# Kernel optimization log

Hardware: AMD Instinct MI355X
Metric: run time of the kernel (lower is better)

## Reference

```python
import jax, jax.numpy as jnp
import numpy as np

HID, FFN, E, K = 1024, 4096, 8, 2
CAP_FACTOR = 1.25


def setup_inputs() -> dict:
    key = jax.random.key(0)
    k1, k2, k3, k4 = jax.random.split(key, 4)
    B, T = 4, 2048
    x = jax.random.normal(k1, (B, T, HID), dtype=jnp.float32)
    router_w = jax.random.normal(k2, (E, HID), dtype=jnp.float32) * 0.02
    w1 = jax.random.normal(k3, (E, HID, FFN), dtype=jnp.float32) * 0.02
    w2 = jax.random.normal(k4, (E, FFN, HID), dtype=jnp.float32) * 0.02
    return {"x": x, "router_w": router_w, "w1": w1, "w2": w2}


def reference(x, router_w, w1, w2):
    B, T, H = x.shape
    N = B * T
    x_flat = x.reshape(N, H)
    # capacity per expert (static, shape-derived)
    C = max(1, int(CAP_FACTOR * N / E * K))

    # router (eval mode: no noise)
    logits = x_flat @ router_w.T                      # [N, E]
    probs = jax.nn.softmax(logits, axis=-1)
    top_v, top_i = jax.lax.top_k(probs, K)            # [N, K]
    top_v = top_v / jnp.sum(top_v, axis=-1, keepdims=True)

    out = jnp.zeros_like(x_flat)
    for k in range(K):
        eid = top_i[:, k]                             # [N] expert id per token
        gate = top_v[:, k]                            # [N]
        # position of each token within its expert, in token order
        onehot = jax.nn.one_hot(eid, E, dtype=jnp.int32)          # [N, E]
        pos = jnp.take_along_axis(jnp.cumsum(onehot, axis=0), eid[:, None], axis=1)[:, 0] - 1
        keep = pos < C                                # capacity drop (first C in token order)
        slot = jnp.where(keep, eid * C + pos, E * C)  # dropped tokens -> dump slot

        # dispatch: scatter kept tokens into per-expert capacity buffers
        buf = jnp.zeros((E * C + 1, H), dtype=x.dtype).at[slot].add(
            x_flat * keep[:, None].astype(x.dtype))
        expert_in = buf[: E * C].reshape(E, C, H)     # [E, C, H]

        # per-expert FFN (grouped GEMM -> GELU -> grouped GEMM)
        h = jax.nn.gelu(jnp.einsum('ech,ehf->ecf', expert_in, w1), approximate=False)
        y = jnp.einsum('ecf,efh->ech', h, w2)         # [E, C, H]

        # combine: gather back to token order, mask dropped, apply gate
        tok = y.reshape(E * C, H)[jnp.minimum(slot, E * C - 1)]
        out = out + tok * (gate * keep.astype(x.dtype))[:, None]

    return out.reshape(B, T, H)
```

## Files before the change

kernel.cpp:

```cpp
#include <hip/hip_runtime.h>
#include <hip/hip_bf16.h>
#include <math.h>

#define N_TOK 8192
#define HIDD  1024
#define FFND  4096
#define NE    8
#define CAP   2560
#define TMX   20
#define RMAX  16512

typedef __attribute__((ext_vector_type(4))) float  f32x4;
typedef __attribute__((ext_vector_type(8))) __bf16 bf16x8;

__device__ __forceinline__ unsigned short f2bf(float f) {
    unsigned u = __float_as_uint(f);
    u = (u + 0x7fffu + ((u >> 16) & 1u)) >> 16;
    return (unsigned short)u;
}

__device__ __forceinline__ void gld_lds16(const void* g, void* l) {
    __builtin_amdgcn_global_load_lds(
        (const __attribute__((address_space(1))) unsigned int*)g,
        (__attribute__((address_space(3))) unsigned int*)l, 16, 0, 0);
}

template <int R, int C>
__global__ __launch_bounds__(256) void transpose_cvt(const float* __restrict__ W,
                                                     unsigned short* __restrict__ Wt) {
    __shared__ unsigned short st[64][72];
    int e  = blockIdx.z;
    int r0 = blockIdx.y * 64, c0 = blockIdx.x * 64;
    int tid = threadIdx.x;
    int rb = tid >> 4, cq = tid & 15;
    const float* src = W + ((size_t)e * R + r0) * C + c0;
#pragma unroll
    for (int i = 0; i < 4; i++) {
        int kr = i * 16 + rb;
        float4 v = *reinterpret_cast<const float4*>(src + (size_t)kr * C + cq * 4);
        st[cq * 4 + 0][kr] = f2bf(v.x);
        st[cq * 4 + 1][kr] = f2bf(v.y);
        st[cq * 4 + 2][kr] = f2bf(v.z);
        st[cq * 4 + 3][kr] = f2bf(v.w);
    }
    __syncthreads();
    unsigned short* dst = Wt + ((size_t)e * C + c0) * R + r0;
#pragma unroll
    for (int i = 0; i < 4; i++) {
        int cr = i * 16 + rb;
        uint2 v = *reinterpret_cast<const uint2*>(&st[cr][cq * 4]);
        *reinterpret_cast<uint2*>(dst + (size_t)cr * R + cq * 4) = v;
    }
}

__global__ __launch_bounds__(256) void router_kernel(const float* __restrict__ x,
                                                     const float* __restrict__ rw,
                                                     unsigned short* __restrict__ xbf,
                                                     int* __restrict__ cnt,
                                                     int* __restrict__ tok,
                                                     float* __restrict__ gate) {
    __shared__ float4 rwl[2048];
    __shared__ int   e0s[32], e1s[32];
    __shared__ float g0s[32], g1s[32];
    __shared__ int   baseS[16];

    int tid = threadIdx.x, lane = tid & 63, w = tid >> 6;
    for (int i = tid; i < 2048; i += 256) rwl[i] = reinterpret_cast<const float4*>(rw)[i];
    __syncthreads();

    int tbase = blockIdx.x * 32 + w * 8;
    for (int i = 0; i < 8; i++) {
        int t = tbase + i;
        const float4* xr = reinterpret_cast<const float4*>(x) + (size_t)t * 256;
        float4 xv[4];
#pragma unroll
        for (int c = 0; c < 4; c++) xv[c] = xr[c * 64 + lane];
        uint2* xb = reinterpret_cast<uint2*>(xbf) + (size_t)t * 256;
#pragma unroll
        for (int c = 0; c < 4; c++) {
            uint2 p;
            p.x = (unsigned)f2bf(xv[c].x) | ((unsigned)f2bf(xv[c].y) << 16);
            p.y = (unsigned)f2bf(xv[c].z) | ((unsigned)f2bf(xv[c].w) << 16);
            xb[c * 64 + lane] = p;
        }
        float dot[NE];
#pragma unroll
        for (int e = 0; e < NE; e++) {
            float s = 0.f;
#pragma unroll
            for (int c = 0; c < 4; c++) {
                float4 a = rwl[e * 256 + c * 64 + lane];
                s += xv[c].x * a.x + xv[c].y * a.y + xv[c].z * a.z + xv[c].w * a.w;
            }
            dot[e] = s;
        }
#pragma unroll
        for (int e = 0; e < NE; e++) {
            float v = dot[e];
#pragma unroll
            for (int o = 32; o > 0; o >>= 1) v += __shfl_xor(v, o, 64);
            dot[e] = v;
        }
        if (lane == 0) {
            int e0 = 0; float l0 = dot[0];
#pragma unroll
            for (int e = 1; e < NE; e++) if (dot[e] > l0) { l0 = dot[e]; e0 = e; }
            int e1 = -1; float l1 = -3.4e38f;
#pragma unroll
            for (int e = 0; e < NE; e++) if (e != e0 && dot[e] > l1) { l1 = dot[e]; e1 = e; }
            float g0 = 1.f / (1.f + expf(l1 - l0));
            int j = w * 8 + i;
            e0s[j] = e0; e1s[j] = e1; g0s[j] = g0; g1s[j] = 1.f - g0;
        }
    }
    __syncthreads();

    int e0 = 255, e1 = 255, rank0 = 0, rank1 = 0, slotcnt = 0;
    float g0 = 0.f, g1 = 0.f;
    if (w == 0) {
        if (lane < 32) { e0 = e0s[lane]; e1 = e1s[lane]; g0 = g0s[lane]; g1 = g1s[lane]; }
        unsigned long long lt = (1ull << lane) - 1ull;
#pragma unroll
        for (int ee = 0; ee < NE; ee++) {
            unsigned long long m0 = __ballot(e0 == ee);
            unsigned long long m1 = __ballot(e1 == ee);
            if (e0 == ee) rank0 = (int)__popcll(m0 & lt);
            if (e1 == ee) rank1 = (int)__popcll(m1 & lt);
            if (lane == ee)      slotcnt = (int)__popcll(m0);
            if (lane == NE + ee) slotcnt = (int)__popcll(m1);
        }
        if (lane < 16) baseS[lane] = atomicAdd(&cnt[lane * 16], slotcnt);
    }
    __syncthreads();
    if (w == 0 && lane < 32) {
        int t = blockIdx.x * 32 + lane;
        int p0 = baseS[e0] + rank0;
        if (p0 < CAP) { tok[e0 * CAP + p0] = t; gate[e0 * CAP + p0] = g0; }
        int p1 = baseS[NE + e1] + rank1;
        if (p1 < CAP) { tok[(NE + e1) * CAP + p1] = t; gate[(NE + e1) * CAP + p1] = g1; }
    }
}

template <int KD, int ND, bool G1, int CH>
__global__ __launch_bounds__(256) void ffn_gemm_f(const unsigned short* __restrict__ A,
                                                  const unsigned short* __restrict__ Bw,
                                                  unsigned short* __restrict__ H,
                                                  float* __restrict__ O,
                                                  const int* __restrict__ cntAll,
                                                  const int* __restrict__ tokL,
                                                  const float* __restrict__ gateL) {
    constexpr int TN = ND / 128;
    int e = blockIdx.x & 7;
    int i = blockIdx.x >> 3;
    int cnt0 = min(cntAll[e * 16], CAP);
    int cnt1 = min(cntAll[(e + 8) * 16], CAP);
    int tmx0 = (cnt0 + 127) >> 7;
    int tmx1 = (cnt1 + 127) >> 7;
    int tmsum = tmx0 + tmx1;
    if (tmsum == 0) return;
    int per_chunk = tmsum * CH;
    int c = i / per_chunk;
    if (c >= TN / CH) return;
    int r = i - c * per_chunk;
    int s, tm, cnt_e;
    int t0 = tmx0 * CH;
    if (r < t0) { s = e;     tm = r / CH; r -= tm * CH; cnt_e = cnt0; }
    else { r -= t0; s = e + 8; tm = r / CH; r -= tm * CH; cnt_e = cnt1; }
    int tn = c * CH + r;

    int off_e = 0;
#pragma unroll
    for (int t = 0; t < 16; t++) off_e += (t < s) ? min(cntAll[t * 16], CAP) : 0;
    const int lbase = s * CAP;

    __shared__ __align__(16) unsigned short At[128 * 32];
    __shared__ __align__(16) unsigned short Bt[128 * 32];

    int tid = threadIdx.x;
    int w = tid >> 6, l = tid & 63;
    int wr = w >> 1, wc = w & 1;

    int r1 = tid >> 2, q1 = tid & 3;
    int r2 = r1 + 64;

    const char* aSrc1;
    const char* aSrc2;
    if (G1) {
        int p1 = tm * 128 + r1, p2 = tm * 128 + r2;
        int t1 = tokL[lbase + (p1 < cnt_e ? p1 : 0)];
        int t2 = tokL[lbase + (p2 < cnt_e ? p2 : 0)];
        aSrc1 = (const char*)(A + (size_t)t1 * KD) + ((q1 ^ ((r1 >> 1) & 3)) << 4);
        aSrc2 = (const char*)(A + (size_t)t2 * KD) + ((q1 ^ ((r2 >> 1) & 3)) << 4);
    } else {
        size_t row1 = (size_t)off_e + tm * 128 + r1;
        size_t row2 = row1 + 64;
        aSrc1 = (const char*)(A + row1 * KD) + ((q1 ^ ((r1 >> 1) & 3)) << 4);
        aSrc2 = (const char*)(A + row2 * KD) + ((q1 ^ ((r2 >> 1) & 3)) << 4);
    }
    const char* bSrc1 = (const char*)(Bw + ((size_t)e * ND + tn * 128 + r1) * KD) + ((q1 ^ ((r1 >> 1) & 3)) << 4);
    const char* bSrc2 = (const char*)(Bw + ((size_t)e * ND + tn * 128 + r2) * KD) + ((q1 ^ ((r2 >> 1) & 3)) << 4);

    char* aDst1 = (char*)At + w * 1024;
    char* aDst2 = aDst1 + 4096;
    char* bDst1 = (char*)Bt + w * 1024;
    char* bDst2 = bDst1 + 4096;

    int aro[4], bro[4];
#pragma unroll
    for (int m = 0; m < 4; m++) {
        int rr = wr * 64 + m * 16 + (l & 15);
        aro[m] = rr * 64 + (((l >> 4) ^ ((rr >> 1) & 3)) << 4);
        int cc = wc * 64 + m * 16 + (l & 15);
        bro[m] = cc * 64 + (((l >> 4) ^ ((cc >> 1) & 3)) << 4);
    }

    f32x4 zf = {0.f, 0.f, 0.f, 0.f};
    f32x4 acc[4][4];
#pragma unroll
    for (int m = 0; m < 4; m++)
#pragma unroll
        for (int n = 0; n < 4; n++) acc[m][n] = zf;

    for (int k0 = 0; k0 < KD; k0 += 32) {
        size_t kb = (size_t)k0 * 2;
        gld_lds16(aSrc1 + kb, aDst1);
        gld_lds16(aSrc2 + kb, aDst2);
        gld_lds16(bSrc1 + kb, bDst1);
        gld_lds16(bSrc2 + kb, bDst2);
        __syncthreads();
        bf16x8 af[4], bf[4];
#pragma unroll
        for (int m = 0; m < 4; m++) af[m] = *reinterpret_cast<const bf16x8*>((const char*)At + aro[m]);
#pragma unroll
        for (int n = 0; n < 4; n++) bf[n] = *reinterpret_cast<const bf16x8*>((const char*)Bt + bro[n]);
#pragma unroll
        for (int m = 0; m < 4; m++)
#pragma unroll
            for (int n = 0; n < 4; n++)
                acc[m][n] = __builtin_amdgcn_mfma_f32_16x16x32_bf16(af[m], bf[n], acc[m][n], 0, 0, 0);
        __syncthreads();
    }

    if (G1) {
#pragma unroll
        for (int m = 0; m < 4; m++) {
#pragma unroll
            for (int j = 0; j < 4; j++) {
                int rr = wr * 64 + m * 16 + (l >> 4) * 4 + j;
                int p = tm * 128 + rr;
                if (p < cnt_e) {
                    size_t row = (size_t)(off_e + p);
                    unsigned short* hp = H + row * ND + tn * 128 + wc * 64 + (l & 15);
#pragma unroll
                    for (int n = 0; n < 4; n++) {
                        float v = acc[m][n][j];
                        float g = 0.5f * v * (1.f + erff(v * 0.70710678118654752f));
                        hp[n * 16] = f2bf(g);
                    }
                }
            }
        }
    } else {
#pragma unroll
        for (int m = 0; m < 4; m++) {
#pragma unroll
            for (int j = 0; j < 4; j++) {
                int rr = wr * 64 + m * 16 + (l >> 4) * 4 + j;
                int p = tm * 128 + rr;
                if (p < cnt_e) {
                    int t = tokL[lbase + p];
                    float gv = gateL[lbase + p];
                    float* op = O + (size_t)t * ND + tn * 128 + wc * 64 + (l & 15);
#pragma unroll
                    for (int n = 0; n < 4; n++) atomicAdd(op + n * 16, gv * acc[m][n][j]);
                }
            }
        }
    }
}

template <int KD, int ND, bool G1>
__global__ __launch_bounds__(256) void ffn_gemm(const unsigned short* __restrict__ A,
                                                const float* __restrict__ W,
                                                unsigned short* __restrict__ H,
                                                float* __restrict__ O,
                                                const int* __restrict__ cntAll,
                                                const int* __restrict__ tokL,
                                                const float* __restrict__ gateL,
                                                int slot0, int pbase) {
    constexpr int TN = ND / 128;
    int bid = blockIdx.x;
    int tn  = bid % TN;
    int tme = bid / TN;
    int tm  = tme % TMX;
    int s   = slot0 + tme / TMX;
    int eW  = s & 7;
    int cnt_e = min(cntAll[s * 16], CAP);
    if (tm * 128 >= cnt_e) return;
    int off_e = 0;
#pragma unroll
    for (int i = 0; i < 16; i++) {
        int c = min(cntAll[i * 16], CAP);
        off_e += (i >= pbase && i < s) ? c : 0;
    }
    const int lbase = s * CAP;

    __shared__ __align__(16) unsigned short At[128 * 32];
    __shared__ __align__(16) unsigned short Bt[128 * 32];

    int tid = threadIdx.x;
    int w = tid >> 6, l = tid & 63;
    int wr = w >> 1, wc = w & 1;

    int r1 = tid >> 2, q1 = tid & 3;
    int r2 = r1 + 64;
    const char* aSrc1;
    const char* aSrc2;
    if (G1) {
        int p1 = tm * 128 + r1, p2 = tm * 128 + r2;
        int t1 = tokL[lbase + (p1 < cnt_e ? p1 : 0)];
        int t2 = tokL[lbase + (p2 < cnt_e ? p2 : 0)];
        aSrc1 = (const char*)(A + (size_t)t1 * KD) + ((q1 ^ ((r1 >> 1) & 3)) << 4);
        aSrc2 = (const char*)(A + (size_t)t2 * KD) + ((q1 ^ ((r2 >> 1) & 3)) << 4);
    } else {
        size_t row1 = (size_t)off_e + tm * 128 + r1;
        size_t row2 = row1 + 64;
        aSrc1 = (const char*)(A + row1 * KD) + ((q1 ^ ((r1 >> 1) & 3)) << 4);
        aSrc2 = (const char*)(A + row2 * KD) + ((q1 ^ ((r2 >> 1) & 3)) << 4);
    }
    char* aDst1 = (char*)At + w * 1024;
    char* aDst2 = aDst1 + 4096;

    const float* bSrc[4];
    int bOff[16];
#pragma unroll
    for (int j = 0; j < 4; j++) {
        int fidx = j * 1024 + tid * 4;
        int kk = fidx >> 7, n = fidx & 127;
        bSrc[j] = W + (size_t)eW * KD * ND + (size_t)kk * ND + tn * 128 + n;
#pragma unroll
        for (int i = 0; i < 4; i++) {
            int nn = n + i;
            bOff[j * 4 + i] = nn * 64 + ((((kk >> 3) ^ ((nn >> 1) & 3))) << 4) + ((kk & 7) << 1);
        }
    }

    int aro[4], bro[4];
#pragma unroll
    for (int m = 0; m < 4; m++) {
        int rr = wr * 64 + m * 16 + (l & 15);
        aro[m] = rr * 64 + (((l >> 4) ^ ((rr >> 1) & 3)) << 4);
        int cc = wc * 64 + m * 16 + (l & 15);
        bro[m] = cc * 64 + (((l >> 4) ^ ((cc >> 1) & 3)) << 4);
    }

    f32x4 zf = {0.f, 0.f, 0.f, 0.f};
    f32x4 acc[4][4];
#pragma unroll
    for (int m = 0; m < 4; m++)
#pragma unroll
        for (int n = 0; n < 4; n++) acc[m][n] = zf;

    for (int k0 = 0; k0 < KD; k0 += 32) {
        gld_lds16(aSrc1 + (size_t)k0 * 2, aDst1);
        gld_lds16(aSrc2 + (size_t)k0 * 2, aDst2);
        float4 bv[4];
#pragma unroll
        for (int j = 0; j < 4; j++) bv[j] = *reinterpret_cast<const float4*>(bSrc[j] + (size_t)k0 * ND);
        char* btc = (char*)Bt;
#pragma unroll
        for (int j = 0; j < 4; j++) {
            *(unsigned short*)(btc + bOff[j * 4 + 0]) = f2bf(bv[j].x);
            *(unsigned short*)(btc + bOff[j * 4 + 1]) = f2bf(bv[j].y);
            *(unsigned short*)(btc + bOff[j * 4 + 2]) = f2bf(bv[j].z);
            *(unsigned short*)(btc + bOff[j * 4 + 3]) = f2bf(bv[j].w);
        }
        __syncthreads();
        bf16x8 af[4], bf[4];
#pragma unroll
        for (int m = 0; m < 4; m++) af[m] = *reinterpret_cast<const bf16x8*>((const char*)At + aro[m]);
#pragma unroll
        for (int n = 0; n < 4; n++) bf[n] = *reinterpret_cast<const bf16x8*>((const char*)Bt + bro[n]);
#pragma unroll
        for (int m = 0; m < 4; m++)
#pragma unroll
            for (int n = 0; n < 4; n++)
                acc[m][n] = __builtin_amdgcn_mfma_f32_16x16x32_bf16(af[m], bf[n], acc[m][n], 0, 0, 0);
        __syncthreads();
    }

    if (G1) {
#pragma unroll
        for (int m = 0; m < 4; m++) {
#pragma unroll
            for (int j = 0; j < 4; j++) {
                int rr = wr * 64 + m * 16 + (l >> 4) * 4 + j;
                int p = tm * 128 + rr;
                if (p < cnt_e) {
                    size_t row = (size_t)(off_e + p);
                    unsigned short* hp = H + row * ND + tn * 128 + wc * 64 + (l & 15);
#pragma unroll
                    for (int n = 0; n < 4; n++) {
                        float v = acc[m][n][j];
                        float g = 0.5f * v * (1.f + erff(v * 0.70710678118654752f));
                        hp[n * 16] = f2bf(g);
                    }
                }
            }
        }
    } else {
#pragma unroll
        for (int m = 0; m < 4; m++) {
#pragma unroll
            for (int j = 0; j < 4; j++) {
                int rr = wr * 64 + m * 16 + (l >> 4) * 4 + j;
                int p = tm * 128 + rr;
                if (p < cnt_e) {
                    int t = tokL[lbase + p];
                    float gv = gateL[lbase + p];
                    float* op = O + (size_t)t * ND + tn * 128 + wc * 64 + (l & 15);
#pragma unroll
                    for (int n = 0; n < 4; n++) atomicAdd(op + n * 16, gv * acc[m][n][j]);
                }
            }
        }
    }
}

extern "C" void kernel_launch(void* const* d_in, const int* in_sizes, int n_in,
                              void* d_out, int out_size, void* d_ws, size_t ws_size,
                              hipStream_t stream) {
    const float* x  = (const float*)d_in[0];
    const float* rw = (const float*)d_in[1];
    const float* w1 = (const float*)d_in[2];
    const float* w2 = (const float*)d_in[3];
    float* out = (float*)d_out;
    char* ws = (char*)d_ws;

    int*   cnt  = (int*)ws;
    int*   tok  = (int*)(ws + 4096);
    float* gate = (float*)(ws + 4096 + 16 * CAP * 4);
    unsigned short* xbf = (unsigned short*)(ws + (1 << 20));
    size_t hOff = (1 << 20) + (size_t)N_TOK * HIDD * 2;
    unsigned short* h = (unsigned short*)(ws + hOff);

    size_t w1tSz = (size_t)NE * HIDD * FFND * 2;
    size_t hBig = (size_t)RMAX * FFND * 2;
    size_t needBig = hOff + hBig + 2 * w1tSz;

    hipMemsetAsync(cnt, 0, 1024, stream);
    hipMemsetAsync(d_out, 0, (size_t)N_TOK * HIDD * 4, stream);

    hipLaunchKernelGGL(router_kernel, dim3(N_TOK / 32), dim3(256), 0, stream,
                       x, rw, xbf, cnt, tok, gate);

    if (ws_size >= needBig) {
        unsigned short* w1t = (unsigned short*)(ws + hOff + hBig);
        unsigned short* w2t = (unsigned short*)(ws + hOff + hBig + w1tSz);
        hipLaunchKernelGGL((transpose_cvt<HIDD, FFND>), dim3(FFND / 64, HIDD / 64, NE), dim3(256), 0, stream, w1, w1t);
        hipLaunchKernelGGL((transpose_cvt<FFND, HIDD>), dim3(HIDD / 64, FFND / 64, NE), dim3(256), 0, stream, w2, w2t);
        hipLaunchKernelGGL((ffn_gemm_f<HIDD, FFND, true, 8>), dim3(8 * 2 * TMX * (FFND / 128)), dim3(256), 0, stream,
                           xbf, w1t, h, (float*)nullptr, cnt, tok, gate);
        hipLaunchKernelGGL((ffn_gemm_f<FFND, HIDD, false, 4>), dim3(8 * 2 * TMX * (HIDD / 128)), dim3(256), 0, stream,
                           h, w2t, (unsigned short*)nullptr, out, cnt, tok, gate);
    } else {
        for (int k = 0; k < 2; k++) {
            hipLaunchKernelGGL((ffn_gemm<HIDD, FFND, true>), dim3(8 * TMX * (FFND / 128)), dim3(256), 0, stream,
                               xbf, w1, h, (float*)nullptr, cnt, tok, gate, 8 * k, 8 * k);
            hipLaunchKernelGGL((ffn_gemm<FFND, HIDD, false>), dim3(8 * TMX * (HIDD / 128)), dim3(256), 0, stream,
                               h, w2, (unsigned short*)nullptr, out, cnt, tok, gate, 8 * k, 8 * k);
        }
    }
}
```

Baseline: 558.8 us.

## Replace expert GEMMs with 256-row tiled, double-buffered 8-wave kernel with split-K

```diff
diff --git a/kernel.cpp b/kernel.cpp
--- a/kernel.cpp
+++ b/kernel.cpp
@@ -8,6 +8,7 @@
 #define NE    8
 #define CAP   2560
 #define TMX   20
+#define TMX2  10
 #define RMAX  16512
 
 typedef __attribute__((ext_vector_type(4))) float  f32x4;
@@ -141,118 +142,183 @@
     }
 }
 
-template <int KD, int ND, bool G1, int CH>
-__global__ __launch_bounds__(256) void ffn_gemm_f(const unsigned short* __restrict__ A,
-                                                  const unsigned short* __restrict__ Bw,
-                                                  unsigned short* __restrict__ H,
-                                                  float* __restrict__ O,
-                                                  const int* __restrict__ cntAll,
-                                                  const int* __restrict__ tokL,
-                                                  const float* __restrict__ gateL) {
-    constexpr int TN = ND / 128;
+template <int KD, int ND, int BN, int KS, bool G1>
+__global__ __launch_bounds__(512, 2) void ffn_gemm8(const unsigned short* __restrict__ A,
+                                                    const unsigned short* __restrict__ Bw,
+                                                    unsigned short* __restrict__ H,
+                                                    float* __restrict__ O,
+                                                    const int* __restrict__ cntAll,
+                                                    const int* __restrict__ tokL,
+                                                    const float* __restrict__ gateL) {
+    constexpr int TN      = ND / BN;
+    constexpr int UNITS   = TN * KS;
+    constexpr int WAVES_M = G1 ? 2 : 4;
+    constexpr int WAVES_N = 8 / WAVES_M;
+    constexpr int M_REP   = 256 / (WAVES_M * 16);
+    constexpr int N_REP   = BN / (WAVES_N * 16);
+    constexpr int BSW     = BN / 64;
+    constexpr int KDS     = KD / KS;
+    constexpr int NT      = KDS / 64;
+    constexpr int LDSA    = 256 * 128;
+    constexpr int LDSB    = BN * 128;
+
+    extern __shared__ __align__(16) char smem[];
+
     int e = blockIdx.x & 7;
     int i = blockIdx.x >> 3;
     int cnt0 = min(cntAll[e * 16], CAP);
     int cnt1 = min(cntAll[(e + 8) * 16], CAP);
-    int tmx0 = (cnt0 + 127) >> 7;
-    int tmx1 = (cnt1 + 127) >> 7;
+    int tmx0 = (cnt0 + 255) >> 8, tmx1 = (cnt1 + 255) >> 8;
     int tmsum = tmx0 + tmx1;
     if (tmsum == 0) return;
-    int per_chunk = tmsum * CH;
+    int per_chunk = tmsum * 4;
     int c = i / per_chunk;
-    if (c >= TN / CH) return;
+    if (c >= UNITS / 4) return;
     int r = i - c * per_chunk;
     int s, tm, cnt_e;
-    int t0 = tmx0 * CH;
-    if (r < t0) { s = e;     tm = r / CH; r -= tm * CH; cnt_e = cnt0; }
-    else { r -= t0; s = e + 8; tm = r / CH; r -= tm * CH; cnt_e = cnt1; }
-    int tn = c * CH + r;
+    if (r < tmx0 * 4) { s = e;     tm = r >> 2; r &= 3; cnt_e = cnt0; }
+    else { r -= tmx0 * 4; s = e + 8; tm = r >> 2; r &= 3; cnt_e = cnt1; }
+    int u  = c * 4 + r;
+    int tn = u / KS, ks = (KS > 1) ? (u % KS) : 0;
 
     int off_e = 0;
 #pragma unroll
     for (int t = 0; t < 16; t++) off_e += (t < s) ? min(cntAll[t * 16], CAP) : 0;
     const int lbase = s * CAP;
 
-    __shared__ __align__(16) unsigned short At[128 * 32];
-    __shared__ __align__(16) unsigned short Bt[128 * 32];
-
     int tid = threadIdx.x;
-    int w = tid >> 6, l = tid & 63;
-    int wr = w >> 1, wc = w & 1;
-
-    int r1 = tid >> 2, q1 = tid & 3;
-    int r2 = r1 + 64;
-
-    const char* aSrc1;
-    const char* aSrc2;
+    int l = tid & 63, w = tid >> 6;
+
+    int srow = w * 8 + (l >> 3);
+    int swz  = (((l & 7) ^ ((l >> 3) & 7)) << 4);
+
+    int aoff[4];
+#pragma unroll
+    for (int j = 0; j < 4; j++) {
+        int p = tm * 256 + j * 64 + srow;
+        if (G1) {
+            int t = tokL[lbase + (p < cnt_e ? p : 0)];
+            aoff[j] = t * (KD * 2) + ks * (KDS * 2) + swz;
+        } else {
+            aoff[j] = (off_e + p) * (KD * 2) + ks * (KDS * 2) + swz;
+        }
+    }
+    int boff[BSW];
+#pragma unroll
+    for (int j = 0; j < BSW; j++) {
+        int nr = e * ND + tn * BN + j * 64 + srow;
+        boff[j] = nr * (KD * 2) + ks * (KDS * 2) + swz;
+    }
+    int dstoff = (w * 8) * 128;
+
+    int wm = G1 ? (w >> 2) : (w >> 1);
+    int wn = G1 ? (w & 3) : (w & 1);
+    int arow = wm * (256 / WAVES_M) + (l & 15);
+    int brow = wn * (BN / WAVES_N) + (l & 15);
+    int rsw  = (((l >> 4) ^ (l & 7)) << 4);
+    int aR[2], bR[2];
+    aR[0] = arow * 128 + rsw;  aR[1] = aR[0] ^ 64;
+    bR[0] = brow * 128 + rsw;  bR[1] = bR[0] ^ 64;
+
+    const char* Ab = (const char*)A;
+    const char* Bb = (const char*)Bw;
+
+    f32x4 acc[M_REP][N_REP];
+#pragma unroll
+    for (int m = 0; m < M_REP; m++)
+#pragma unroll
+        for (int n = 0; n < N_REP; n++) acc[m][n] = (f32x4){0.f, 0.f, 0.f, 0.f};
+
+#pragma unroll
+    for (int j = 0; j < 4; j++)   gld_lds16(Ab + aoff[j], smem + dstoff + j * 8192);
+#pragma unroll
+    for (int j = 0; j < BSW; j++) gld_lds16(Bb + boff[j], smem + LDSA + dstoff + j * 8192);
+#pragma unroll
+    for (int j = 0; j < 4; j++)   aoff[j] += 128;
+#pragma unroll
+    for (int j = 0; j < BSW; j++) boff[j] += 128;
+
+    bf16x8 afr[M_REP][2], bfr[N_REP][2];
+
+    for (int t = 0; t < NT - 1; t++) {
+        char* bufc = smem + (t & 1) * (LDSA + LDSB);
+        char* bufn = smem + ((t + 1) & 1) * (LDSA + LDSB);
+#pragma unroll
+        for (int j = 0; j < 4; j++) { gld_lds16(Ab + aoff[j], bufn + dstoff + j * 8192); aoff[j] += 128; }
+        asm volatile("s_waitcnt vmcnt(4)" ::: "memory");
+        __builtin_amdgcn_s_barrier();
+        asm volatile("" ::: "memory");
+#pragma unroll
+        for (int m = 0; m < M_REP; m++)
+#pragma unroll
+            for (int kk = 0; kk < 2; kk++)
+                afr[m][kk] = *reinterpret_cast<const bf16x8*>(bufc + aR[kk] + m * 2048);
+#pragma unroll
+        for (int n = 0; n < N_REP; n++)
+#pragma unroll
+            for (int kk = 0; kk < 2; kk++)
+                bfr[n][kk] = *reinterpret_cast<const bf16x8*>(bufc + LDSA + bR[kk] + n * 2048);
+        __builtin_amdgcn_s_setprio(1);
+#pragma unroll
+        for (int m = 0; m < M_REP; m++)
+#pragma unroll
+            for (int n = 0; n < N_REP; n++)
+                acc[m][n] = __builtin_amdgcn_mfma_f32_16x16x32_bf16(afr[m][0], bfr[n][0], acc[m][n], 0, 0, 0);
+        __builtin_amdgcn_s_setprio(0);
+#pragma unroll
+        for (int j = 0; j < BSW; j++) { gld_lds16(Bb + boff[j], bufn + LDSA + dstoff + j * 8192); boff[j] += 128; }
+        asm volatile("s_waitcnt lgkmcnt(0)" ::: "memory");
+        __builtin_amdgcn_sched_barrier(0);
+        __builtin_amdgcn_s_barrier();
+        asm volatile("" ::: "memory");
+        __builtin_amdgcn_s_setprio(1);
+#pragma unroll
+        for (int m = 0; m < M_REP; m++)
+#pragma unroll
+            for (int n = 0; n < N_REP; n++)
+                acc[m][n] = __builtin_amdgcn_mfma_f32_16x16x32_bf16(afr[m][1], bfr[n][1], acc[m][n], 0, 0, 0);
+        __builtin_amdgcn_s_setprio(0);
+    }
+    {
+        char* bufc = smem + ((NT - 1) & 1) * (LDSA + LDSB);
+        asm volatile("s_waitcnt vmcnt(0)" ::: "memory");
+        __builtin_amdgcn_s_barrier();
+        asm volatile("" ::: "memory");
+#pragma unroll
+        for (int m = 0; m < M_REP; m++)
+#pragma unroll
+            for (int kk = 0; kk < 2; kk++)
+                afr[m][kk] = *reinterpret_cast<const bf16x8*>(bufc + aR[kk] + m * 2048);
+#pragma unroll
+        for (int n = 0; n < N_REP; n++)
+#pragma unroll
+            for (int kk = 0; kk < 2; kk++)
+                bfr[n][kk] = *reinterpret_cast<const bf16x8*>(bufc + LDSA + bR[kk] + n * 2048);
+        __builtin_amdgcn_s_setprio(1);
+#pragma unroll
+        for (int m = 0; m < M_REP; m++)
+#pragma unroll
+            for (int n = 0; n < N_REP; n++)
+                acc[m][n] = __builtin_amdgcn_mfma_f32_16x16x32_bf16(afr[m][0], bfr[n][0], acc[m][n], 0, 0, 0);
+#pragma unroll
+        for (int m = 0; m < M_REP; m++)
+#pragma unroll
+            for (int n = 0; n < N_REP; n++)
+                acc[m][n] = __builtin_amdgcn_mfma_f32_16x16x32_bf16(afr[m][1], bfr[n][1], acc[m][n], 0, 0, 0);
+        __builtin_amdgcn_s_setprio(0);
+    }
+
     if (G1) {
-        int p1 = tm * 128 + r1, p2 = tm * 128 + r2;
-        int t1 = tokL[lbase + (p1 < cnt_e ? p1 : 0)];
-        int t2 = tokL[lbase + (p2 < cnt_e ? p2 : 0)];
-        aSrc1 = (const char*)(A + (size_t)t1 * KD) + ((q1 ^ ((r1 >> 1) & 3)) << 4);
-        aSrc2 = (const char*)(A + (size_t)t2 * KD) + ((q1 ^ ((r2 >> 1) & 3)) << 4);
-    } else {
-        size_t row1 = (size_t)off_e + tm * 128 + r1;
-        size_t row2 = row1 + 64;
-        aSrc1 = (const char*)(A + row1 * KD) + ((q1 ^ ((r1 >> 1) & 3)) << 4);
-        aSrc2 = (const char*)(A + row2 * KD) + ((q1 ^ ((r2 >> 1) & 3)) << 4);
-    }
-    const char* bSrc1 = (const char*)(Bw + ((size_t)e * ND + tn * 128 + r1) * KD) + ((q1 ^ ((r1 >> 1) & 3)) << 4);
-    const char* bSrc2 = (const char*)(Bw + ((size_t)e * ND + tn * 128 + r2) * KD) + ((q1 ^ ((r2 >> 1) & 3)) << 4);
-
-    char* aDst1 = (char*)At + w * 1024;
-    char* aDst2 = aDst1 + 4096;
-    char* bDst1 = (char*)Bt + w * 1024;
-    char* bDst2 = bDst1 + 4096;
-
-    int aro[4], bro[4];
-#pragma unroll
-    for (int m = 0; m < 4; m++) {
-        int rr = wr * 64 + m * 16 + (l & 15);
-        aro[m] = rr * 64 + (((l >> 4) ^ ((rr >> 1) & 3)) << 4);
-        int cc = wc * 64 + m * 16 + (l & 15);
-        bro[m] = cc * 64 + (((l >> 4) ^ ((cc >> 1) & 3)) << 4);
-    }
-
-    f32x4 zf = {0.f, 0.f, 0.f, 0.f};
-    f32x4 acc[4][4];
-#pragma unroll
-    for (int m = 0; m < 4; m++)
-#pragma unroll
-        for (int n = 0; n < 4; n++) acc[m][n] = zf;
-
-    for (int k0 = 0; k0 < KD; k0 += 32) {
-        size_t kb = (size_t)k0 * 2;
-        gld_lds16(aSrc1 + kb, aDst1);
-        gld_lds16(aSrc2 + kb, aDst2);
-        gld_lds16(bSrc1 + kb, bDst1);
-        gld_lds16(bSrc2 + kb, bDst2);
-        __syncthreads();
-        bf16x8 af[4], bf[4];
-#pragma unroll
-        for (int m = 0; m < 4; m++) af[m] = *reinterpret_cast<const bf16x8*>((const char*)At + aro[m]);
-#pragma unroll
-        for (int n = 0; n < 4; n++) bf[n] = *reinterpret_cast<const bf16x8*>((const char*)Bt + bro[n]);
-#pragma unroll
-        for (int m = 0; m < 4; m++)
-#pragma unroll
-            for (int n = 0; n < 4; n++)
-                acc[m][n] = __builtin_amdgcn_mfma_f32_16x16x32_bf16(af[m], bf[n], acc[m][n], 0, 0, 0);
-        __syncthreads();
-    }
-
-    if (G1) {
-#pragma unroll
-        for (int m = 0; m < 4; m++) {
+#pragma unroll
+        for (int m = 0; m < M_REP; m++) {
 #pragma unroll
             for (int j = 0; j < 4; j++) {
-                int rr = wr * 64 + m * 16 + (l >> 4) * 4 + j;
-                int p = tm * 128 + rr;
+                int rr = wm * (256 / WAVES_M) + m * 16 + (l >> 4) * 4 + j;
+                int p = tm * 256 + rr;
                 if (p < cnt_e) {
-                    size_t row = (size_t)(off_e + p);
-                    unsigned short* hp = H + row * ND + tn * 128 + wc * 64 + (l & 15);
-#pragma unroll
-                    for (int n = 0; n < 4; n++) {
+                    unsigned short* hp = H + (size_t)(off_e + p) * ND + tn * BN + wn * (BN / WAVES_N) + (l & 15);
+#pragma unroll
+                    for (int n = 0; n < N_REP; n++) {
                         float v = acc[m][n][j];
                         float g = 0.5f * v * (1.f + erff(v * 0.70710678118654752f));
                         hp[n * 16] = f2bf(g);
@@ -262,17 +328,17 @@
         }
     } else {
 #pragma unroll
-        for (int m = 0; m < 4; m++) {
+        for (int m = 0; m < M_REP; m++) {
 #pragma unroll
             for (int j = 0; j < 4; j++) {
-                int rr = wr * 64 + m * 16 + (l >> 4) * 4 + j;
-                int p = tm * 128 + rr;
+                int rr = wm * (256 / WAVES_M) + m * 16 + (l >> 4) * 4 + j;
+                int p = tm * 256 + rr;
                 if (p < cnt_e) {
                     int t = tokL[lbase + p];
                     float gv = gateL[lbase + p];
-                    float* op = O + (size_t)t * ND + tn * 128 + wc * 64 + (l & 15);
-#pragma unroll
-                    for (int n = 0; n < 4; n++) atomicAdd(op + n * 16, gv * acc[m][n][j]);
+                    float* op = O + (size_t)t * ND + tn * BN + wn * (BN / WAVES_N) + (l & 15);
+#pragma unroll
+                    for (int n = 0; n < N_REP; n++) atomicAdd(op + n * 16, gv * acc[m][n][j]);
                 }
             }
         }
@@ -459,9 +525,11 @@
         unsigned short* w2t = (unsigned short*)(ws + hOff + hBig + w1tSz);
         hipLaunchKernelGGL((transpose_cvt<HIDD, FFND>), dim3(FFND / 64, HIDD / 64, NE), dim3(256), 0, stream, w1, w1t);
         hipLaunchKernelGGL((transpose_cvt<FFND, HIDD>), dim3(HIDD / 64, FFND / 64, NE), dim3(256), 0, stream, w2, w2t);
-        hipLaunchKernelGGL((ffn_gemm_f<HIDD, FFND, true, 8>), dim3(8 * 2 * TMX * (FFND / 128)), dim3(256), 0, stream,
+        hipLaunchKernelGGL((ffn_gemm8<HIDD, FFND, 256, 1, true>), dim3(8 * 2 * TMX2 * 16), dim3(512),
+                           2 * (256 * 128 + 256 * 128), stream,
                            xbf, w1t, h, (float*)nullptr, cnt, tok, gate);
-        hipLaunchKernelGGL((ffn_gemm_f<FFND, HIDD, false, 4>), dim3(8 * 2 * TMX * (HIDD / 128)), dim3(256), 0, stream,
+        hipLaunchKernelGGL((ffn_gemm8<FFND, HIDD, 128, 2, false>), dim3(8 * 2 * TMX2 * 16), dim3(512),
+                           2 * (256 * 128 + 128 * 128), stream,
                            h, w2t, (unsigned short*)nullptr, out, cnt, tok, gate);
     } else {
         for (int k = 0; k < 2; k++) {
```

Result: slower. 578.0 us (+3.4%).

## Use 256x128 tiles with triple-buffered async LDS pipeline and split-K

Applied to the files above, without the earlier changes.

```diff
diff --git a/kernel.cpp b/kernel.cpp
--- a/kernel.cpp
+++ b/kernel.cpp
@@ -141,116 +141,151 @@
     }
 }
 
-template <int KD, int ND, bool G1, int CH>
-__global__ __launch_bounds__(256) void ffn_gemm_f(const unsigned short* __restrict__ A,
-                                                  const unsigned short* __restrict__ Bw,
-                                                  unsigned short* __restrict__ H,
-                                                  float* __restrict__ O,
-                                                  const int* __restrict__ cntAll,
-                                                  const int* __restrict__ tokL,
-                                                  const float* __restrict__ gateL) {
-    constexpr int TN = ND / 128;
+template <int KD, int ND, int KS, bool G1>
+__global__ __launch_bounds__(512, 2) void ffn_gemm8(const unsigned short* __restrict__ A,
+                                                    const unsigned short* __restrict__ Bw,
+                                                    unsigned short* __restrict__ H,
+                                                    float* __restrict__ O,
+                                                    const int* __restrict__ cntAll,
+                                                    const int* __restrict__ tokL,
+                                                    const float* __restrict__ gateL) {
+    constexpr int TN    = ND / 128;
+    constexpr int UNITS = TN * KS;
+    constexpr int CH    = G1 ? 8 : 4;
+    constexpr int KDS   = KD / KS;
+    constexpr int NT    = KDS / 64;
+    constexpr int LDSA  = 256 * 128;
+    constexpr int LDSB  = 128 * 128;
+    constexpr int BUF   = LDSA + LDSB;
+
+    extern __shared__ __align__(16) char smem[];
+
     int e = blockIdx.x & 7;
     int i = blockIdx.x >> 3;
     int cnt0 = min(cntAll[e * 16], CAP);
     int cnt1 = min(cntAll[(e + 8) * 16], CAP);
-    int tmx0 = (cnt0 + 127) >> 7;
-    int tmx1 = (cnt1 + 127) >> 7;
+    int tmx0 = (cnt0 + 255) >> 8, tmx1 = (cnt1 + 255) >> 8;
     int tmsum = tmx0 + tmx1;
     if (tmsum == 0) return;
     int per_chunk = tmsum * CH;
     int c = i / per_chunk;
-    if (c >= TN / CH) return;
+    if (c >= UNITS / CH) return;
     int r = i - c * per_chunk;
     int s, tm, cnt_e;
-    int t0 = tmx0 * CH;
-    if (r < t0) { s = e;     tm = r / CH; r -= tm * CH; cnt_e = cnt0; }
-    else { r -= t0; s = e + 8; tm = r / CH; r -= tm * CH; cnt_e = cnt1; }
-    int tn = c * CH + r;
+    if (r < tmx0 * CH) { s = e;     tm = r / CH; r -= tm * CH; cnt_e = cnt0; }
+    else { r -= tmx0 * CH; s = e + 8; tm = r / CH; r -= tm * CH; cnt_e = cnt1; }
+    int u  = c * CH + r;
+    int tn = (KS > 1) ? (u / KS) : u;
+    int ks = (KS > 1) ? (u % KS) : 0;
 
     int off_e = 0;
 #pragma unroll
     for (int t = 0; t < 16; t++) off_e += (t < s) ? min(cntAll[t * 16], CAP) : 0;
     const int lbase = s * CAP;
 
-    __shared__ __align__(16) unsigned short At[128 * 32];
-    __shared__ __align__(16) unsigned short Bt[128 * 32];
-
     int tid = threadIdx.x;
-    int w = tid >> 6, l = tid & 63;
-    int wr = w >> 1, wc = w & 1;
-
-    int r1 = tid >> 2, q1 = tid & 3;
-    int r2 = r1 + 64;
-
-    const char* aSrc1;
-    const char* aSrc2;
-    if (G1) {
-        int p1 = tm * 128 + r1, p2 = tm * 128 + r2;
-        int t1 = tokL[lbase + (p1 < cnt_e ? p1 : 0)];
-        int t2 = tokL[lbase + (p2 < cnt_e ? p2 : 0)];
-        aSrc1 = (const char*)(A + (size_t)t1 * KD) + ((q1 ^ ((r1 >> 1) & 3)) << 4);
-        aSrc2 = (const char*)(A + (size_t)t2 * KD) + ((q1 ^ ((r2 >> 1) & 3)) << 4);
-    } else {
-        size_t row1 = (size_t)off_e + tm * 128 + r1;
-        size_t row2 = row1 + 64;
-        aSrc1 = (const char*)(A + row1 * KD) + ((q1 ^ ((r1 >> 1) & 3)) << 4);
-        aSrc2 = (const char*)(A + row2 * KD) + ((q1 ^ ((r2 >> 1) & 3)) << 4);
-    }
-    const char* bSrc1 = (const char*)(Bw + ((size_t)e * ND + tn * 128 + r1) * KD) + ((q1 ^ ((r1 >> 1) & 3)) << 4);
-    const char* bSrc2 = (const char*)(Bw + ((size_t)e * ND + tn * 128 + r2) * KD) + ((q1 ^ ((r2 >> 1) & 3)) << 4);
-
-    char* aDst1 = (char*)At + w * 1024;
-    char* aDst2 = aDst1 + 4096;
-    char* bDst1 = (char*)Bt + w * 1024;
-    char* bDst2 = bDst1 + 4096;
-
-    int aro[4], bro[4];
-#pragma unroll
-    for (int m = 0; m < 4; m++) {
-        int rr = wr * 64 + m * 16 + (l & 15);
-        aro[m] = rr * 64 + (((l >> 4) ^ ((rr >> 1) & 3)) << 4);
-        int cc = wc * 64 + m * 16 + (l & 15);
-        bro[m] = cc * 64 + (((l >> 4) ^ ((cc >> 1) & 3)) << 4);
-    }
-
-    f32x4 zf = {0.f, 0.f, 0.f, 0.f};
+    int l = tid & 63, w = tid >> 6;
+
+    int srow = w * 8 + (l >> 3);
+    int swz  = (((l & 7) ^ ((l >> 3) & 7)) << 4);
+
+    int aoff[4];
+#pragma unroll
+    for (int j = 0; j < 4; j++) {
+        int p = tm * 256 + j * 64 + srow;
+        if (G1) {
+            int t = tokL[lbase + (p < cnt_e ? p : 0)];
+            aoff[j] = t * (KD * 2) + ks * (KDS * 2) + swz;
+        } else {
+            aoff[j] = (off_e + p) * (KD * 2) + ks * (KDS * 2) + swz;
+        }
+    }
+    int boff[2];
+#pragma unroll
+    for (int j = 0; j < 2; j++) {
+        int nr = e * ND + tn * 128 + j * 64 + srow;
+        boff[j] = nr * (KD * 2) + ks * (KDS * 2) + swz;
+    }
+    int adst = w * 1024;
+
+    const char* Ab = (const char*)A;
+    const char* Bb = (const char*)Bw;
+
+    int wm = w >> 1, wn = w & 1;
+    int arow = wm * 64 + (l & 15);
+    int brow = wn * 64 + (l & 15);
+    int rsw  = (((l >> 4) ^ (l & 7)) << 4);
+    int aR0 = arow * 128 + rsw;
+    int bR0 = brow * 128 + rsw;
+
     f32x4 acc[4][4];
 #pragma unroll
     for (int m = 0; m < 4; m++)
 #pragma unroll
-        for (int n = 0; n < 4; n++) acc[m][n] = zf;
-
-    for (int k0 = 0; k0 < KD; k0 += 32) {
-        size_t kb = (size_t)k0 * 2;
-        gld_lds16(aSrc1 + kb, aDst1);
-        gld_lds16(aSrc2 + kb, aDst2);
-        gld_lds16(bSrc1 + kb, bDst1);
-        gld_lds16(bSrc2 + kb, bDst2);
-        __syncthreads();
+        for (int n = 0; n < 4; n++) acc[m][n] = (f32x4){0.f, 0.f, 0.f, 0.f};
+
+    char* b0 = smem;
+    char* b1 = smem + BUF;
+    char* b2 = smem + 2 * BUF;
+
+#define STAGE_A(buf) do { _Pragma("unroll") \
+    for (int j = 0; j < 4; j++) { gld_lds16(Ab + aoff[j], (buf) + adst + j * 8192); aoff[j] += 128; } } while (0)
+#define STAGE_B(buf) do { _Pragma("unroll") \
+    for (int j = 0; j < 2; j++) { gld_lds16(Bb + boff[j], (buf) + LDSA + adst + j * 8192); boff[j] += 128; } } while (0)
+
+    STAGE_A(b0); STAGE_B(b0);
+    STAGE_A(b1); STAGE_B(b1);
+    asm volatile("s_waitcnt vmcnt(6)" ::: "memory");
+    __builtin_amdgcn_s_barrier();
+    asm volatile("" ::: "memory");
+
+    for (int t = 0; t < NT; t++) {
+        bool pf = (t + 2 < NT);
         bf16x8 af[4], bf[4];
 #pragma unroll
-        for (int m = 0; m < 4; m++) af[m] = *reinterpret_cast<const bf16x8*>((const char*)At + aro[m]);
-#pragma unroll
-        for (int n = 0; n < 4; n++) bf[n] = *reinterpret_cast<const bf16x8*>((const char*)Bt + bro[n]);
+        for (int m = 0; m < 4; m++) af[m] = *reinterpret_cast<const bf16x8*>(b0 + aR0 + m * 2048);
+#pragma unroll
+        for (int n = 0; n < 4; n++) bf[n] = *reinterpret_cast<const bf16x8*>(b0 + LDSA + bR0 + n * 2048);
+        if (pf) STAGE_A(b2);
+        __builtin_amdgcn_s_setprio(1);
 #pragma unroll
         for (int m = 0; m < 4; m++)
 #pragma unroll
             for (int n = 0; n < 4; n++)
                 acc[m][n] = __builtin_amdgcn_mfma_f32_16x16x32_bf16(af[m], bf[n], acc[m][n], 0, 0, 0);
-        __syncthreads();
-    }
+        __builtin_amdgcn_s_setprio(0);
+#pragma unroll
+        for (int m = 0; m < 4; m++) af[m] = *reinterpret_cast<const bf16x8*>(b0 + (aR0 ^ 64) + m * 2048);
+#pragma unroll
+        for (int n = 0; n < 4; n++) bf[n] = *reinterpret_cast<const bf16x8*>(b0 + LDSA + (bR0 ^ 64) + n * 2048);
+        if (pf) STAGE_B(b2);
+        __builtin_amdgcn_s_setprio(1);
+#pragma unroll
+        for (int m = 0; m < 4; m++)
+#pragma unroll
+            for (int n = 0; n < 4; n++)
+                acc[m][n] = __builtin_amdgcn_mfma_f32_16x16x32_bf16(af[m], bf[n], acc[m][n], 0, 0, 0);
+        __builtin_amdgcn_s_setprio(0);
+        if (pf) asm volatile("s_waitcnt vmcnt(6)" ::: "memory");
+        else    asm volatile("s_waitcnt vmcnt(0)" ::: "memory");
+        if (t + 1 < NT) {
+            __builtin_amdgcn_s_barrier();
+            asm volatile("" ::: "memory");
+        }
+        char* bt = b0; b0 = b1; b1 = b2; b2 = bt;
+    }
+#undef STAGE_A
+#undef STAGE_B
 
     if (G1) {
 #pragma unroll
         for (int m = 0; m < 4; m++) {
 #pragma unroll
             for (int j = 0; j < 4; j++) {
-                int rr = wr * 64 + m * 16 + (l >> 4) * 4 + j;
-                int p = tm * 128 + rr;
+                int rr = wm * 64 + m * 16 + (l >> 4) * 4 + j;
+                int p = tm * 256 + rr;
                 if (p < cnt_e) {
-                    size_t row = (size_t)(off_e + p);
-                    unsigned short* hp = H + row * ND + tn * 128 + wc * 64 + (l & 15);
+                    unsigned short* hp = H + (size_t)(off_e + p) * ND + tn * 128 + wn * 64 + (l & 15);
 #pragma unroll
                     for (int n = 0; n < 4; n++) {
                         float v = acc[m][n][j];
@@ -265,12 +300,12 @@
         for (int m = 0; m < 4; m++) {
 #pragma unroll
             for (int j = 0; j < 4; j++) {
-                int rr = wr * 64 + m * 16 + (l >> 4) * 4 + j;
-                int p = tm * 128 + rr;
+                int rr = wm * 64 + m * 16 + (l >> 4) * 4 + j;
+                int p = tm * 256 + rr;
                 if (p < cnt_e) {
                     int t = tokL[lbase + p];
                     float gv = gateL[lbase + p];
-                    float* op = O + (size_t)t * ND + tn * 128 + wc * 64 + (l & 15);
+                    float* op = O + (size_t)t * ND + tn * 128 + wn * 64 + (l & 15);
 #pragma unroll
                     for (int n = 0; n < 4; n++) atomicAdd(op + n * 16, gv * acc[m][n][j]);
                 }
@@ -459,10 +494,11 @@
         unsigned short* w2t = (unsigned short*)(ws + hOff + hBig + w1tSz);
         hipLaunchKernelGGL((transpose_cvt<HIDD, FFND>), dim3(FFND / 64, HIDD / 64, NE), dim3(256), 0, stream, w1, w1t);
         hipLaunchKernelGGL((transpose_cvt<FFND, HIDD>), dim3(HIDD / 64, FFND / 64, NE), dim3(256), 0, stream, w2, w2t);
-        hipLaunchKernelGGL((ffn_gemm_f<HIDD, FFND, true, 8>), dim3(8 * 2 * TMX * (FFND / 128)), dim3(256), 0, stream,
-                           xbf, w1t, h, (float*)nullptr, cnt, tok, gate);
-        hipLaunchKernelGGL((ffn_gemm_f<FFND, HIDD, false, 4>), dim3(8 * 2 * TMX * (HIDD / 128)), dim3(256), 0, stream,
-                           h, w2t, (unsigned short*)nullptr, out, cnt, tok, gate);
+        constexpr int SMEM = 3 * (256 * 128 + 128 * 128);
+        hipLaunchKernelGGL((ffn_gemm8<HIDD, FFND, 1, true>), dim3(8 * 20 * 32), dim3(512),
+                           SMEM, stream, xbf, w1t, h, (float*)nullptr, cnt, tok, gate);
+        hipLaunchKernelGGL((ffn_gemm8<FFND, HIDD, 2, false>), dim3(8 * 20 * 16), dim3(512),
+                           SMEM, stream, h, w2t, (unsigned short*)nullptr, out, cnt, tok, gate);
     } else {
         for (int k = 0; k < 2; k++) {
             hipLaunchKernelGGL((ffn_gemm<HIDD, FFND, true>), dim3(8 * TMX * (FFND / 128)), dim3(256), 0, stream,
```

New measurement: 572.1 us. 2.4% more time.

## Use persistent per-expert GEMM blocks and split-K for the second FFN GEMM

Applied to the files above, without the earlier changes.

```diff
diff --git a/kernel.cpp b/kernel.cpp
--- a/kernel.cpp
+++ b/kernel.cpp
@@ -9,6 +9,7 @@
 #define CAP   2560
 #define TMX   20
 #define RMAX  16512
+#define PBLK  128
 
 typedef __attribute__((ext_vector_type(4))) float  f32x4;
 typedef __attribute__((ext_vector_type(8))) __bf16 bf16x8;
@@ -141,40 +142,39 @@
     }
 }
 
-template <int KD, int ND, bool G1, int CH>
-__global__ __launch_bounds__(256) void ffn_gemm_f(const unsigned short* __restrict__ A,
-                                                  const unsigned short* __restrict__ Bw,
-                                                  unsigned short* __restrict__ H,
-                                                  float* __restrict__ O,
-                                                  const int* __restrict__ cntAll,
-                                                  const int* __restrict__ tokL,
-                                                  const float* __restrict__ gateL) {
-    constexpr int TN = ND / 128;
-    int e = blockIdx.x & 7;
-    int i = blockIdx.x >> 3;
+template <int KD, int ND, int KS, int CH, bool G1>
+__global__ __launch_bounds__(256, 4) void ffn_gemm_p(const unsigned short* __restrict__ A,
+                                                     const unsigned short* __restrict__ Bw,
+                                                     unsigned short* __restrict__ H,
+                                                     float* __restrict__ O,
+                                                     const int* __restrict__ cntAll,
+                                                     const int* __restrict__ tokL,
+                                                     const float* __restrict__ gateL) {
+    constexpr int TN    = ND / 128;
+    constexpr int UNITS = TN * KS;
+    constexpr int KDS   = KD / KS;
+
+    __shared__ __align__(16) unsigned short At[128 * 32];
+    __shared__ __align__(16) unsigned short Bt[128 * 32];
+
+    int e  = blockIdx.x & 7;
+    int pb = blockIdx.x >> 3;
+
     int cnt0 = min(cntAll[e * 16], CAP);
     int cnt1 = min(cntAll[(e + 8) * 16], CAP);
-    int tmx0 = (cnt0 + 127) >> 7;
-    int tmx1 = (cnt1 + 127) >> 7;
+    int tmx0 = (cnt0 + 127) >> 7, tmx1 = (cnt1 + 127) >> 7;
     int tmsum = tmx0 + tmx1;
     if (tmsum == 0) return;
     int per_chunk = tmsum * CH;
-    int c = i / per_chunk;
-    if (c >= TN / CH) return;
-    int r = i - c * per_chunk;
-    int s, tm, cnt_e;
-    int t0 = tmx0 * CH;
-    if (r < t0) { s = e;     tm = r / CH; r -= tm * CH; cnt_e = cnt0; }
-    else { r -= t0; s = e + 8; tm = r / CH; r -= tm * CH; cnt_e = cnt1; }
-    int tn = c * CH + r;
-
-    int off_e = 0;
-#pragma unroll
-    for (int t = 0; t < 16; t++) off_e += (t < s) ? min(cntAll[t * 16], CAP) : 0;
-    const int lbase = s * CAP;
-
-    __shared__ __align__(16) unsigned short At[128 * 32];
-    __shared__ __align__(16) unsigned short Bt[128 * 32];
+    int total = tmsum * UNITS;
+
+    int offA = 0, offB = 0;
+#pragma unroll
+    for (int t = 0; t < 16; t++) {
+        int cc = min(cntAll[t * 16], CAP);
+        if (t < e)     offA += cc;
+        if (t < e + 8) offB += cc;
+    }
 
     int tid = threadIdx.x;
     int w = tid >> 6, l = tid & 63;
@@ -182,24 +182,8 @@
 
     int r1 = tid >> 2, q1 = tid & 3;
     int r2 = r1 + 64;
-
-    const char* aSrc1;
-    const char* aSrc2;
-    if (G1) {
-        int p1 = tm * 128 + r1, p2 = tm * 128 + r2;
-        int t1 = tokL[lbase + (p1 < cnt_e ? p1 : 0)];
-        int t2 = tokL[lbase + (p2 < cnt_e ? p2 : 0)];
-        aSrc1 = (const char*)(A + (size_t)t1 * KD) + ((q1 ^ ((r1 >> 1) & 3)) << 4);
-        aSrc2 = (const char*)(A + (size_t)t2 * KD) + ((q1 ^ ((r2 >> 1) & 3)) << 4);
-    } else {
-        size_t row1 = (size_t)off_e + tm * 128 + r1;
-        size_t row2 = row1 + 64;
-        aSrc1 = (const char*)(A + row1 * KD) + ((q1 ^ ((r1 >> 1) & 3)) << 4);
-        aSrc2 = (const char*)(A + row2 * KD) + ((q1 ^ ((r2 >> 1) & 3)) << 4);
-    }
-    const char* bSrc1 = (const char*)(Bw + ((size_t)e * ND + tn * 128 + r1) * KD) + ((q1 ^ ((r1 >> 1) & 3)) << 4);
-    const char* bSrc2 = (const char*)(Bw + ((size_t)e * ND + tn * 128 + r2) * KD) + ((q1 ^ ((r2 >> 1) & 3)) << 4);
-
+    int sw1 = ((q1 ^ ((r1 >> 1) & 3)) << 4);
+    int sw2 = ((q1 ^ ((r2 >> 1) & 3)) << 4);
     char* aDst1 = (char*)At + w * 1024;
     char* aDst2 = aDst1 + 4096;
     char* bDst1 = (char*)Bt + w * 1024;
@@ -214,65 +198,91 @@
         bro[m] = cc * 64 + (((l >> 4) ^ ((cc >> 1) & 3)) << 4);
     }
 
-    f32x4 zf = {0.f, 0.f, 0.f, 0.f};
-    f32x4 acc[4][4];
-#pragma unroll
-    for (int m = 0; m < 4; m++)
-#pragma unroll
-        for (int n = 0; n < 4; n++) acc[m][n] = zf;
-
-    for (int k0 = 0; k0 < KD; k0 += 32) {
-        size_t kb = (size_t)k0 * 2;
-        gld_lds16(aSrc1 + kb, aDst1);
-        gld_lds16(aSrc2 + kb, aDst2);
-        gld_lds16(bSrc1 + kb, bDst1);
-        gld_lds16(bSrc2 + kb, bDst2);
-        __syncthreads();
-        bf16x8 af[4], bf[4];
-#pragma unroll
-        for (int m = 0; m < 4; m++) af[m] = *reinterpret_cast<const bf16x8*>((const char*)At + aro[m]);
-#pragma unroll
-        for (int n = 0; n < 4; n++) bf[n] = *reinterpret_cast<const bf16x8*>((const char*)Bt + bro[n]);
+    for (int u0 = pb; u0 < total; u0 += PBLK) {
+        int c = u0 / per_chunk;
+        int r = u0 - c * per_chunk;
+        int s, tm, cnt_e, off_e;
+        if (r < tmx0 * CH) { s = e;     tm = r / CH; r -= tm * CH; cnt_e = cnt0; off_e = offA; }
+        else { r -= tmx0 * CH; s = e + 8; tm = r / CH; r -= tm * CH; cnt_e = cnt1; off_e = offB; }
+        int u  = c * CH + r;
+        int tn = (KS > 1) ? (u / KS) : u;
+        int ks = (KS > 1) ? (u % KS) : 0;
+        const int lbase = s * CAP;
+
+        const char* aSrc1;
+        const char* aSrc2;
+        if (G1) {
+            int p1 = tm * 128 + r1, p2 = tm * 128 + r2;
+            int t1 = tokL[lbase + (p1 < cnt_e ? p1 : 0)];
+            int t2 = tokL[lbase + (p2 < cnt_e ? p2 : 0)];
+            aSrc1 = (const char*)(A + (size_t)t1 * KD + ks * KDS) + sw1;
+            aSrc2 = (const char*)(A + (size_t)t2 * KD + ks * KDS) + sw2;
+        } else {
+            size_t row1 = (size_t)off_e + tm * 128 + r1;
+            aSrc1 = (const char*)(A + row1 * KD + ks * KDS) + sw1;
+            aSrc2 = (const char*)(A + (row1 + 64) * KD + ks * KDS) + sw2;
+        }
+        const char* bSrc1 = (const char*)(Bw + ((size_t)e * ND + tn * 128 + r1) * KD + ks * KDS) + sw1;
+        const char* bSrc2 = (const char*)(Bw + ((size_t)e * ND + tn * 128 + r2) * KD + ks * KDS) + sw2;
+
+        f32x4 acc[4][4];
 #pragma unroll
         for (int m = 0; m < 4; m++)
 #pragma unroll
-            for (int n = 0; n < 4; n++)
-                acc[m][n] = __builtin_amdgcn_mfma_f32_16x16x32_bf16(af[m], bf[n], acc[m][n], 0, 0, 0);
-        __syncthreads();
-    }
-
-    if (G1) {
-#pragma unroll
-        for (int m = 0; m < 4; m++) {
-#pragma unroll
-            for (int j = 0; j < 4; j++) {
-                int rr = wr * 64 + m * 16 + (l >> 4) * 4 + j;
-                int p = tm * 128 + rr;
-                if (p < cnt_e) {
-                    size_t row = (size_t)(off_e + p);
-                    unsigned short* hp = H + row * ND + tn * 128 + wc * 64 + (l & 15);
-#pragma unroll
-                    for (int n = 0; n < 4; n++) {
-                        float v = acc[m][n][j];
-                        float g = 0.5f * v * (1.f + erff(v * 0.70710678118654752f));
-                        hp[n * 16] = f2bf(g);
+            for (int n = 0; n < 4; n++) acc[m][n] = (f32x4){0.f, 0.f, 0.f, 0.f};
+
+        for (int k0 = 0; k0 < KDS; k0 += 32) {
+            size_t kb = (size_t)k0 * 2;
+            gld_lds16(aSrc1 + kb, aDst1);
+            gld_lds16(aSrc2 + kb, aDst2);
+            gld_lds16(bSrc1 + kb, bDst1);
+            gld_lds16(bSrc2 + kb, bDst2);
+            __syncthreads();
+            bf16x8 af[4], bf[4];
+#pragma unroll
+            for (int m = 0; m < 4; m++) af[m] = *reinterpret_cast<const bf16x8*>((const char*)At + aro[m]);
+#pragma unroll
+            for (int n = 0; n < 4; n++) bf[n] = *reinterpret_cast<const bf16x8*>((const char*)Bt + bro[n]);
+#pragma unroll
+            for (int m = 0; m < 4; m++)
+#pragma unroll
+                for (int n = 0; n < 4; n++)
+                    acc[m][n] = __builtin_amdgcn_mfma_f32_16x16x32_bf16(af[m], bf[n], acc[m][n], 0, 0, 0);
+            __syncthreads();
+        }
+
+        if (G1) {
+#pragma unroll
+            for (int m = 0; m < 4; m++) {
+#pragma unroll
+                for (int j = 0; j < 4; j++) {
+                    int rr = wr * 64 + m * 16 + (l >> 4) * 4 + j;
+                    int p = tm * 128 + rr;
+                    if (p < cnt_e) {
+                        unsigned short* hp = H + (size_t)(off_e + p) * ND + tn * 128 + wc * 64 + (l & 15);
+#pragma unroll
+                        for (int n = 0; n < 4; n++) {
+                            float v = acc[m][n][j];
+                            float g = 0.5f * v * (1.f + erff(v * 0.70710678118654752f));
+                            hp[n * 16] = f2bf(g);
+                        }
                     }
                 }
             }
-        }
-    } else {
-#pragma unroll
-        for (int m = 0; m < 4; m++) {
-#pragma unroll
-            for (int j = 0; j < 4; j++) {
-                int rr = wr * 64 + m * 16 + (l >> 4) * 4 + j;
-                int p = tm * 128 + rr;
-                if (p < cnt_e) {
-                    int t = tokL[lbase + p];
-                    float gv = gateL[lbase + p];
-                    float* op = O + (size_t)t * ND + tn * 128 + wc * 64 + (l & 15);
-#pragma unroll
-                    for (int n = 0; n < 4; n++) atomicAdd(op + n * 16, gv * acc[m][n][j]);
+        } else {
+#pragma unroll
+            for (int m = 0; m < 4; m++) {
+#pragma unroll
+                for (int j = 0; j < 4; j++) {
+                    int rr = wr * 64 + m * 16 + (l >> 4) * 4 + j;
+                    int p = tm * 128 + rr;
+                    if (p < cnt_e) {
+                        int t = tokL[lbase + p];
+                        float gv = gateL[lbase + p];
+                        float* op = O + (size_t)t * ND + tn * 128 + wc * 64 + (l & 15);
+#pragma unroll
+                        for (int n = 0; n < 4; n++) atomicAdd(op + n * 16, gv * acc[m][n][j]);
+                    }
                 }
             }
         }
@@ -459,9 +469,9 @@
         unsigned short* w2t = (unsigned short*)(ws + hOff + hBig + w1tSz);
         hipLaunchKernelGGL((transpose_cvt<HIDD, FFND>), dim3(FFND / 64, HIDD / 64, NE), dim3(256), 0, stream, w1, w1t);
         hipLaunchKernelGGL((transpose_cvt<FFND, HIDD>), dim3(HIDD / 64, FFND / 64, NE), dim3(256), 0, stream, w2, w2t);
-        hipLaunchKernelGGL((ffn_gemm_f<HIDD, FFND, true, 8>), dim3(8 * 2 * TMX * (FFND / 128)), dim3(256), 0, stream,
+        hipLaunchKernelGGL((ffn_gemm_p<HIDD, FFND, 1, 8, true>), dim3(8 * PBLK), dim3(256), 0, stream,
                            xbf, w1t, h, (float*)nullptr, cnt, tok, gate);
-        hipLaunchKernelGGL((ffn_gemm_f<FFND, HIDD, false, 4>), dim3(8 * 2 * TMX * (HIDD / 128)), dim3(256), 0, stream,
+        hipLaunchKernelGGL((ffn_gemm_p<FFND, HIDD, 2, 4, false>), dim3(8 * PBLK), dim3(256), 0, stream,
                            h, w2t, (unsigned short*)nullptr, out, cnt, tok, gate);
     } else {
         for (int k = 0; k < 2; k++) {
```

New measurement: 542.1 us. -3.0%, faster.
